# Kernel tuning notes

Measured on AMD Instinct MI355X. Metric: run time of the kernel, lower is better.

Reference implementation:

```python
import jax, jax.numpy as jnp
import numpy as np

# ---- static config (matches init_kwargs) ----
IMG = 56        # num_patches = image_size // patch_size = 112 // 2
WIN = 7         # window_size
SHIFT = 3       # shift_size
C = 256         # projection_dim
H = 8           # num_heads
DH = C // H     # head dim = 32
S = WIN * WIN   # tokens per window = 49
NY = IMG // WIN # windows per side = 8
NW = NY * NY    # windows per image = 64
NMLP = 1024
EPS = 1e-5
SCALE = DH ** (-0.5)


def _relative_position_index():
    ch, cw = np.meshgrid(np.arange(WIN), np.arange(WIN), indexing='ij')
    coords = np.stack([ch, cw]).reshape(2, -1)                 # [2, S]
    rel = coords[:, :, None] - coords[:, None, :]              # [2, S, S]
    rel = rel.transpose(1, 2, 0) + (WIN - 1)                   # [S, S, 2]
    idx = rel[:, :, 0] * (2 * WIN - 1) + rel[:, :, 1]          # [S, S]
    return idx.reshape(-1)                                     # [S*S]

REL_IDX = jnp.asarray(_relative_position_index(), dtype=jnp.int32)


def _attn_mask():
    # Faithful replication of the module's mask construction (incl. the empty
    h_slices = (slice(0, -WIN), slice(-WIN, -SHIFT), slice(-SHIFT, None))
    w_slices = (slice(0, -WIN), slice(-WIN, -WIN), slice(-SHIFT, None))
    m = np.zeros((IMG, IMG), dtype=np.float32)
    count = 0
    for hs in h_slices:
        for ws in w_slices:
            m[hs, ws] = count
            count += 1
    mw = m.reshape(NY, WIN, NY, WIN).transpose(0, 2, 1, 3).reshape(NW, S)
    diff = mw[:, None, :] - mw[:, :, None]
    return np.where(diff != 0, -100.0, 0.0).astype(np.float32)  # [NW, S, S]

ATTN_MASK = jnp.asarray(_attn_mask())


def _layernorm(x, gamma, beta):
    mu = jnp.mean(x, axis=-1, keepdims=True)
    var = jnp.mean(jnp.square(x - mu), axis=-1, keepdims=True)
    return (x - mu) * jax.lax.rsqrt(var + EPS) * gamma + beta


def setup_inputs() -> dict:
    key = jax.random.key(0)
    ks = jax.random.split(key, 12)
    B = 32
    s = lambda fan: 1.0 / np.sqrt(fan)
    return {
        'x': jax.random.normal(ks[0], (B, IMG * IMG, C), dtype=jnp.float32),
        'norm_gamma': jnp.ones((C,), jnp.float32),
        'norm_beta': jnp.zeros((C,), jnp.float32),
        'qkv_w': jax.random.normal(ks[1], (C, 3 * C), jnp.float32) * s(C),
        'qkv_b': jnp.zeros((3 * C,), jnp.float32),
        'proj_w': jax.random.normal(ks[2], (C, C), jnp.float32) * s(C),
        'proj_b': jnp.zeros((C,), jnp.float32),
        'rel_bias_table': jax.random.truncated_normal(ks[3], -2.0, 2.0, ((2 * WIN - 1) ** 2, H), jnp.float32) * 0.02,
        'mlp_w1': jax.random.normal(ks[4], (C, NMLP), jnp.float32) * s(C),
        'mlp_b1': jnp.zeros((NMLP,), jnp.float32),
        'mlp_w2': jax.random.normal(ks[5], (NMLP, C), jnp.float32) * s(NMLP),
        'mlp_b2': jnp.zeros((C,), jnp.float32),
    }


def reference(x, norm_gamma, norm_beta, qkv_w, qkv_b, proj_w, proj_b,
              rel_bias_table, mlp_w1, mlp_b1, mlp_w2, mlp_b2):
    B = x.shape[0]
    # ---- shifted-window attention block ----
    shortcut = x
    xn = _layernorm(x, norm_gamma, norm_beta).reshape(B, IMG, IMG, C)
    shifted = jnp.roll(xn, shift=(-SHIFT, -SHIFT), axis=(1, 2))
    # window partition -> [B*NW, S, C]
    xw = shifted.reshape(B, NY, WIN, NY, WIN, C).transpose(0, 1, 3, 2, 4, 5)
    xw = xw.reshape(B * NW, S, C)
    qkv = xw @ qkv_w + qkv_b                                    # [BnW, S, 3C]
    qkv = qkv.reshape(B * NW, S, 3, H, DH).transpose(2, 0, 3, 1, 4)
    q, k, v = qkv[0] * SCALE, qkv[1], qkv[2]                    # [BnW, H, S, DH]
    attn = jnp.einsum('whsd,whtd->whst', q, k)                  # [BnW, H, S, S]
    bias = rel_bias_table[REL_IDX].reshape(S, S, H).transpose(2, 0, 1)
    attn = attn + bias[None]
    attn = attn.reshape(B, NW, H, S, S) + ATTN_MASK[None, :, None]
    attn = jax.nn.softmax(attn.reshape(B * NW, H, S, S), axis=-1)
    out = jnp.einsum('whst,whtd->wshd', attn, v).reshape(B * NW, S, C)
    out = out @ proj_w + proj_b
    # window reverse + unshift
    out = out.reshape(B, NY, NY, WIN, WIN, C).transpose(0, 1, 3, 2, 4, 5)
    out = out.reshape(B, IMG, IMG, C)
    out = jnp.roll(out, shift=(SHIFT, SHIFT), axis=(1, 2)).reshape(B, IMG * IMG, C)
    x = shortcut + out
    # ---- MLP block (same LayerNorm weights reused, as in original) ----
    shortcut2 = x
    xn2 = _layernorm(x, norm_gamma, norm_beta)
    h = jax.nn.gelu(xn2 @ mlp_w1 + mlp_b1, approximate=False)
    h = h @ mlp_w2 + mlp_b2
    return shortcut2 + h
```

## Files before the change

kernel.cpp:

```cpp
#include <hip/hip_runtime.h>
#include <math.h>

#define IMG   56
#define WINSZ 7
#define SHIFTSZ 3
#define CDIM  256
#define NH    8
#define DH    32
#define SEQ   49
#define NYW   8
#define NWIN  64
#define NMLP  1024
#define BATCH 32
#define NTOK  (BATCH*IMG*IMG)
#define BNW   (BATCH*NWIN)
#define SZT   ((size_t)NTOK*CDIM)
#define QSCALE 0.17677669529663687f
#define EPSLN 1e-5f

typedef __attribute__((ext_vector_type(8))) short short8;
typedef __attribute__((ext_vector_type(4))) float f32x4;

__device__ __forceinline__ float bf2f(unsigned short u) {
    union { unsigned i; float f; } c; c.i = ((unsigned)u) << 16; return c.f;
}
__device__ __forceinline__ unsigned short f2bf(float f) {
    union { float f; unsigned i; } c; c.f = f;
    unsigned r = c.i + 0x7fffu + ((c.i >> 16) & 1u);
    return (unsigned short)(r >> 16);
}

__device__ __forceinline__ float gelu_f(float v) {
    float u = v * 0.70710678118654752f;
    float x = fabsf(u);
    float t = __builtin_amdgcn_rcpf(fmaf(0.3275911f, x, 1.0f));
    float e = __expf(-u * u);
    float p = fmaf(1.061405429f, t, -1.453152027f);
    p = fmaf(p, t, 1.421413741f);
    p = fmaf(p, t, -0.284496736f);
    p = fmaf(p, t, 0.254829592f);
    float er = 1.0f - p * t * e;
    er = copysignf(er, u);
    return 0.5f * v * (1.0f + er);
}

#define GLL16(gp, lp) __builtin_amdgcn_global_load_lds( \
    (__attribute__((address_space(1))) void*)(gp),      \
    (__attribute__((address_space(3))) void*)(lp), 16, 0, 0)

__global__ __launch_bounds__(256) void wtrans(const float* __restrict__ in,
                                              unsigned short* __restrict__ out,
                                              int K, int N) {
    int idx = blockIdx.x * 256 + threadIdx.x;
    if (idx >= K * N) return;
    int n = idx / K, k = idx - n * K;
    out[idx] = f2bf(in[(size_t)k * N + n]);
}

template<int WINDOWED>
__global__ __launch_bounds__(256) void ln_kernel(const float* __restrict__ x,
                                                 const float* __restrict__ gamma,
                                                 const float* __restrict__ beta,
                                                 unsigned short* __restrict__ out) {
    int wave = threadIdx.x >> 6;
    int lane = threadIdx.x & 63;
    int tok  = blockIdx.x * 4 + wave;
    int src  = tok;
    if (WINDOWED) {
        int b  = tok / (NWIN * SEQ);
        int r  = tok - b * (NWIN * SEQ);
        int wl = r / SEQ, s = r - wl * SEQ;
        int wy = wl >> 3, wx = wl & 7;
        int i  = s / WINSZ, j = s - i * WINSZ;
        int hp = wy * WINSZ + i + SHIFTSZ; if (hp >= IMG) hp -= IMG;
        int wp = wx * WINSZ + j + SHIFTSZ; if (wp >= IMG) wp -= IMG;
        src = b * (IMG * IMG) + hp * IMG + wp;
    }
    float4 v = *(const float4*)(x + (size_t)src * CDIM + lane * 4);
    float sum = v.x + v.y + v.z + v.w;
    float ss  = v.x*v.x + v.y*v.y + v.z*v.z + v.w*v.w;
#pragma unroll
    for (int off = 32; off; off >>= 1) {
        sum += __shfl_xor(sum, off);
        ss  += __shfl_xor(ss,  off);
    }
    float mu   = sum * (1.0f / CDIM);
    float var  = ss * (1.0f / CDIM) - mu * mu;
    float rstd = rsqrtf(var + EPSLN);
    float4 g  = *(const float4*)(gamma + lane * 4);
    float4 be = *(const float4*)(beta  + lane * 4);
    ushort4 o;
    o.x = f2bf((v.x - mu) * rstd * g.x + be.x);
    o.y = f2bf((v.y - mu) * rstd * g.y + be.y);
    o.z = f2bf((v.z - mu) * rstd * g.z + be.z);
    o.w = f2bf((v.w - mu) * rstd * g.w + be.w);
    *(ushort4*)(out + (size_t)tok * CDIM + lane * 4) = o;
}

#define EPI_QKV  0
#define EPI_PROJ 1
#define EPI_MLP1 2
#define EPI_MLP2 3

template<int EPI>
__global__ __launch_bounds__(256)
void gemm_bt(const unsigned short* __restrict__ A,
             const unsigned short* __restrict__ Bt,
             int K,
             const float* __restrict__ bias,
             const float* __restrict__ resin,
             float* __restrict__ outF,
             unsigned short* __restrict__ outH) {
    __shared__ __align__(16) unsigned short As[128 * 32];
    __shared__ __align__(16) unsigned short Bs[128 * 32];
    int tid  = threadIdx.x;
    int lane = tid & 63, wave = tid >> 6;
    int q4   = lane >> 4, l16 = lane & 15;
    int wm   = wave >> 1, wn = wave & 1;
    int rowBase = blockIdx.y * 128;
    int colBase = blockIdx.x * 128;

    f32x4 acc[4][4];
#pragma unroll
    for (int i = 0; i < 4; i++)
#pragma unroll
        for (int j = 0; j < 4; j++) acc[i][j] = (f32x4){0.f, 0.f, 0.f, 0.f};

    const unsigned short* Ab = A  + (size_t)rowBase * K;
    const unsigned short* Bb = Bt + (size_t)colBase * K;

    int r0 = wave * 32;
    int ra = r0 + (lane >> 2);
    int rb = ra + 16;
    int ca = (lane & 3) ^ ((ra >> 1) & 3);
    int cb = (lane & 3) ^ ((rb >> 1) & 3);
    const size_t off1 = (size_t)ra * K + ca * 8;
    const size_t off2 = (size_t)rb * K + cb * 8;
    unsigned short* ldsA1 = &As[r0 * 32];
    unsigned short* ldsA2 = &As[(r0 + 16) * 32];
    unsigned short* ldsB1 = &Bs[r0 * 32];
    unsigned short* ldsB2 = &Bs[(r0 + 16) * 32];

    for (int k0 = 0; k0 < K; k0 += 32) {
        __syncthreads();
        GLL16(Ab + off1 + k0, ldsA1);
        GLL16(Ab + off2 + k0, ldsA2);
        GLL16(Bb + off1 + k0, ldsB1);
        GLL16(Bb + off2 + k0, ldsB2);
        __syncthreads();
        short8 af[4], bf[4];
#pragma unroll
        for (int mi = 0; mi < 4; mi++) {
            int r = wm * 64 + mi * 16 + l16;
            af[mi] = *(const short8*)&As[r * 32 + ((q4 ^ ((r >> 1) & 3)) * 8)];
        }
#pragma unroll
        for (int ni = 0; ni < 4; ni++) {
            int r = wn * 64 + ni * 16 + l16;
            bf[ni] = *(const short8*)&Bs[r * 32 + ((q4 ^ ((r >> 1) & 3)) * 8)];
        }
#pragma unroll
        for (int mi = 0; mi < 4; mi++)
#pragma unroll
            for (int ni = 0; ni < 4; ni++)
                acc[mi][ni] = __builtin_amdgcn_mfma_f32_16x16x32_bf16(
                    bf[ni], af[mi], acc[mi][ni], 0, 0, 0);
    }

    int mb = rowBase + wm * 64;
    int nb = colBase + wn * 64;
    float4 bias4[4];
#pragma unroll
    for (int ni = 0; ni < 4; ni++)
        bias4[ni] = *(const float4*)(bias + nb + ni * 16 + q4 * 4);

    if (EPI == EPI_QKV) {
        int three = colBase >> 8;
#pragma unroll
        for (int mi = 0; mi < 4; mi++) {
            int m = mb + mi * 16 + l16;
            int w = m / SEQ, s = m - w * SEQ;
#pragma unroll
            for (int ni = 0; ni < 4; ni++) {
                int n0 = nb + ni * 16 + q4 * 4;
                int hh = (n0 >> 5) & 7, dd0 = n0 & 31;
                const float* bp = (const float*)&bias4[ni];
                if (three == 2) {
#pragma unroll
                    for (int r = 0; r < 4; r++)
                        outH[2 * SZT + (((size_t)(w * NH + hh)) * DH + dd0 + r) * 64 + s] =
                            f2bf(acc[mi][ni][r] + bp[r]);
                } else {
                    float sc = (three == 0) ? QSCALE : 1.0f;
                    ushort4 o;
                    o.x = f2bf((acc[mi][ni][0] + bp[0]) * sc);
                    o.y = f2bf((acc[mi][ni][1] + bp[1]) * sc);
                    o.z = f2bf((acc[mi][ni][2] + bp[2]) * sc);
                    o.w = f2bf((acc[mi][ni][3] + bp[3]) * sc);
                    *(ushort4*)(outH + (size_t)three * SZT +
                                (((size_t)(w * NH + hh)) * SEQ + s) * DH + dd0) = o;
                }
            }
        }
    } else if (EPI == EPI_PROJ) {
#pragma unroll
        for (int mi = 0; mi < 4; mi++) {
            int m = mb + mi * 16 + l16;
            int w = m / SEQ, s = m - w * SEQ;
            int b = w >> 6, wl = w & 63;
            int wy = wl >> 3, wx = wl & 7;
            int ii = s / WINSZ, jj = s - ii * WINSZ;
            int hp = wy * WINSZ + ii + SHIFTSZ; if (hp >= IMG) hp -= IMG;
            int wp = wx * WINSZ + jj + SHIFTSZ; if (wp >= IMG) wp -= IMG;
            size_t tok = (size_t)b * (IMG * IMG) + hp * IMG + wp;
#pragma unroll
            for (int ni = 0; ni < 4; ni++) {
                int n0 = nb + ni * 16 + q4 * 4;
                float4 res = *(const float4*)(resin + tok * CDIM + n0);
                float4 o;
                o.x = acc[mi][ni][0] + bias4[ni].x + res.x;
                o.y = acc[mi][ni][1] + bias4[ni].y + res.y;
                o.z = acc[mi][ni][2] + bias4[ni].z + res.z;
                o.w = acc[mi][ni][3] + bias4[ni].w + res.w;
                *(float4*)(outF + tok * CDIM + n0) = o;
            }
        }
    } else if (EPI == EPI_MLP1) {
#pragma unroll
        for (int mi = 0; mi < 4; mi++) {
            int m = mb + mi * 16 + l16;
#pragma unroll
            for (int ni = 0; ni < 4; ni++) {
                int n0 = nb + ni * 16 + q4 * 4;
                ushort4 o;
                o.x = f2bf(gelu_f(acc[mi][ni][0] + bias4[ni].x));
                o.y = f2bf(gelu_f(acc[mi][ni][1] + bias4[ni].y));
                o.z = f2bf(gelu_f(acc[mi][ni][2] + bias4[ni].z));
                o.w = f2bf(gelu_f(acc[mi][ni][3] + bias4[ni].w));
                *(ushort4*)(outH + (size_t)m * NMLP + n0) = o;
            }
        }
    } else {
#pragma unroll
        for (int mi = 0; mi < 4; mi++) {
            int m = mb + mi * 16 + l16;
#pragma unroll
            for (int ni = 0; ni < 4; ni++) {
                int n0 = nb + ni * 16 + q4 * 4;
                float4 res = *(const float4*)(resin + (size_t)m * CDIM + n0);
                float4 o;
                o.x = acc[mi][ni][0] + bias4[ni].x + res.x;
                o.y = acc[mi][ni][1] + bias4[ni].y + res.y;
                o.z = acc[mi][ni][2] + bias4[ni].z + res.z;
                o.w = acc[mi][ni][3] + bias4[ni].w + res.w;
                *(float4*)(outF + (size_t)m * CDIM + n0) = o;
            }
        }
    }
}

__global__ __launch_bounds__(256) void attn_mfma(const unsigned short* __restrict__ qb,
                                                 const unsigned short* __restrict__ kb,
                                                 const unsigned short* __restrict__ vT,
                                                 const float* __restrict__ rel_tab,
                                                 unsigned short* __restrict__ outp) {
    __shared__ __align__(16) unsigned short Pl[4][64 * 64];
    __shared__ float tab[4][169];
    int tid  = threadIdx.x;
    int wave = tid >> 6, lane = tid & 63;
    int q4   = lane >> 4, l16 = lane & 15;
    int job  = blockIdx.x * 4 + wave;
    int w    = job >> 3, h = job & 7;

    for (int i = lane; i < 169; i += 64) tab[wave][i] = rel_tab[i * NH + h];

    const unsigned short* qg = qb + (size_t)(w * NH + h) * SEQ * DH;
    const unsigned short* kg = kb + (size_t)(w * NH + h) * SEQ * DH;
    short8 aq[4], bk[4];
#pragma unroll
    for (int mi = 0; mi < 4; mi++)
        aq[mi] = *(const short8*)(qg + (mi * 16 + l16) * DH + q4 * 8);
#pragma unroll
    for (int ni = 0; ni < 4; ni++)
        bk[ni] = *(const short8*)(kg + (ni * 16 + l16) * DH + q4 * 8);

    f32x4 acc[4][4];
#pragma unroll
    for (int i = 0; i < 4; i++)
#pragma unroll
        for (int j = 0; j < 4; j++) acc[i][j] = (f32x4){0.f, 0.f, 0.f, 0.f};
#pragma unroll
    for (int mi = 0; mi < 4; mi++)
#pragma unroll
        for (int ni = 0; ni < 4; ni++)
            acc[mi][ni] = __builtin_amdgcn_mfma_f32_16x16x32_bf16(
                aq[mi], bk[ni], acc[mi][ni], 0, 0, 0);

    int wl = w & 63;
    int wy = wl >> 3, wx = wl & 7;
    bool edge = (wy == 7) || (wx == 7);

    int itv[4], jtv[4], ltv[4];
#pragma unroll
    for (int ni = 0; ni < 4; ni++) {
        int t  = ni * 16 + l16;
        int it = (t * 37) >> 8;
        int jt = t - it * 7;
        itv[ni] = it; jtv[ni] = jt;
        int lab;
        if (wx == 7 && jt < 4) lab = 0;
        else {
            int lh = (wy == 7) ? ((it < 4) ? 1 : 2) : 0;
            lab = lh * 3 + ((wx == 7) ? 2 : 0);
        }
        ltv[ni] = lab;
    }

    float rinv[4][4];
#pragma unroll
    for (int mi = 0; mi < 4; mi++) {
#pragma unroll
        for (int r = 0; r < 4; r++) {
            int s  = mi * 16 + q4 * 4 + r;
            int is = (s * 37) >> 8;
            int js = s - is * 7;
            int lab_s;
            if (wx == 7 && js < 4) lab_s = 0;
            else {
                int lh = (wy == 7) ? ((is < 4) ? 1 : 2) : 0;
                lab_s = lh * 3 + ((wx == 7) ? 2 : 0);
            }
            float vv[4];
#pragma unroll
            for (int ni = 0; ni < 4; ni++) {
                int t = ni * 16 + l16;
                float a = acc[mi][ni][r];
                if (t < SEQ) {
                    int idx = (is - itv[ni] + 6) * 13 + (js - jtv[ni] + 6);
                    idx = idx < 0 ? 0 : (idx > 168 ? 168 : idx);
                    a += tab[wave][idx];
                    if (edge && lab_s != ltv[ni]) a -= 100.0f;
                } else {
                    a = -1e30f;
                }
                vv[ni] = a;
            }
            float mx = fmaxf(fmaxf(vv[0], vv[1]), fmaxf(vv[2], vv[3]));
#pragma unroll
            for (int off = 1; off < 16; off <<= 1) mx = fmaxf(mx, __shfl_xor(mx, off));
            float sm = 0.0f;
            unsigned short pb[4];
#pragma unroll
            for (int ni = 0; ni < 4; ni++) {
                float p = __expf(vv[ni] - mx);
                sm += p;
                pb[ni] = f2bf(p);
            }
#pragma unroll
            for (int off = 1; off < 16; off <<= 1) sm += __shfl_xor(sm, off);
            rinv[mi][r] = 1.0f / sm;
#pragma unroll
            for (int ni = 0; ni < 4; ni++) {
                int t  = ni * 16 + l16;
                int kbk = t >> 3, j = t & 7;
                Pl[wave][s * 64 + ((kbk ^ (s & 7)) * 8) + j] = pb[ni];
            }
        }
    }
    __syncthreads();

    short8 pa[4][2];
#pragma unroll
    for (int mi = 0; mi < 4; mi++)
#pragma unroll
        for (int ks = 0; ks < 2; ks++) {
            int m  = mi * 16 + l16;
            int kbk = ks * 4 + q4;
            pa[mi][ks] = *(const short8*)&Pl[wave][m * 64 + ((kbk ^ (m & 7)) * 8)];
        }
    const unsigned short* vg = vT + (size_t)(w * NH + h) * DH * 64;
    short8 bv[2][2];
#pragma unroll
    for (int n2 = 0; n2 < 2; n2++)
#pragma unroll
        for (int ks = 0; ks < 2; ks++)
            bv[n2][ks] = *(const short8*)(vg + (n2 * 16 + l16) * 64 + ks * 32 + q4 * 8);

    f32x4 o[4][2];
#pragma unroll
    for (int mi = 0; mi < 4; mi++)
#pragma unroll
        for (int n2 = 0; n2 < 2; n2++) o[mi][n2] = (f32x4){0.f, 0.f, 0.f, 0.f};
#pragma unroll
    for (int ks = 0; ks < 2; ks++)
#pragma unroll
        for (int mi = 0; mi < 4; mi++)
#pragma unroll
            for (int n2 = 0; n2 < 2; n2++)
                o[mi][n2] = __builtin_amdgcn_mfma_f32_16x16x32_bf16(
                    pa[mi][ks], bv[n2][ks], o[mi][n2], 0, 0, 0);

#pragma unroll
    for (int mi = 0; mi < 4; mi++)
#pragma unroll
        for (int r = 0; r < 4; r++) {
            int s = mi * 16 + q4 * 4 + r;
            if (s < SEQ) {
#pragma unroll
                for (int n2 = 0; n2 < 2; n2++) {
                    int d = n2 * 16 + l16;
                    outp[((size_t)w * SEQ + s) * CDIM + h * DH + d] =
                        f2bf(o[mi][n2][r] * rinv[mi][r]);
                }
            }
        }
}

extern "C" void kernel_launch(void* const* d_in, const int* in_sizes, int n_in,
                              void* d_out, int out_size, void* d_ws, size_t ws_size,
                              hipStream_t stream) {
    const float* x      = (const float*)d_in[0];
    const float* gamma  = (const float*)d_in[1];
    const float* beta   = (const float*)d_in[2];
    const float* qkv_w  = (const float*)d_in[3];
    const float* qkv_b  = (const float*)d_in[4];
    const float* proj_w = (const float*)d_in[5];
    const float* proj_b = (const float*)d_in[6];
    const float* rel_t  = (const float*)d_in[7];
    const float* mlp_w1 = (const float*)d_in[8];
    const float* mlp_b1 = (const float*)d_in[9];
    const float* mlp_w2 = (const float*)d_in[10];
    const float* mlp_b2 = (const float*)d_in[11];
    float* outp = (float*)d_out;

    const size_t VTSZ = (size_t)BNW * NH * DH * 64;
    unsigned short* xw_bf   = (unsigned short*)d_ws;
    unsigned short* qkv_bf  = xw_bf + SZT;
    unsigned short* attn_bf = qkv_bf + 2 * SZT + VTSZ;
    float*          y1      = (float*)(attn_bf + SZT);
    unsigned short* wt_bf   = (unsigned short*)(y1 + SZT);
    unsigned short* h_bf    = qkv_bf;

    unsigned short* qkvW  = wt_bf;
    unsigned short* projW = qkvW  + 768 * 256;
    unsigned short* mlp1W = projW + 256 * 256;
    unsigned short* mlp2W = mlp1W + 1024 * 256;

    wtrans<<<(768 * 256 + 255) / 256, 256, 0, stream>>>(qkv_w, qkvW, CDIM, 3 * CDIM);
    wtrans<<<(256 * 256 + 255) / 256, 256, 0, stream>>>(proj_w, projW, CDIM, CDIM);
    wtrans<<<(1024 * 256 + 255) / 256, 256, 0, stream>>>(mlp_w1, mlp1W, CDIM, NMLP);
    wtrans<<<(256 * 1024 + 255) / 256, 256, 0, stream>>>(mlp_w2, mlp2W, NMLP, CDIM);

    ln_kernel<1><<<NTOK / 4, 256, 0, stream>>>(x, gamma, beta, xw_bf);
    gemm_bt<EPI_QKV><<<dim3(6, NTOK / 128), 256, 0, stream>>>(
        xw_bf, qkvW, CDIM, qkv_b, nullptr, nullptr, qkv_bf);
    attn_mfma<<<BNW * NH / 4, 256, 0, stream>>>(
        qkv_bf, qkv_bf + SZT, qkv_bf + 2 * SZT, rel_t, attn_bf);
    gemm_bt<EPI_PROJ><<<dim3(2, NTOK / 128), 256, 0, stream>>>(
        attn_bf, projW, CDIM, proj_b, x, y1, nullptr);
    ln_kernel<0><<<NTOK / 4, 256, 0, stream>>>(y1, gamma, beta, xw_bf);
    gemm_bt<EPI_MLP1><<<dim3(8, NTOK / 128), 256, 0, stream>>>(
        xw_bf, mlp1W, CDIM, mlp_b1, nullptr, nullptr, h_bf);
    gemm_bt<EPI_MLP2><<<dim3(2, NTOK / 128), 256, 0, stream>>>(
        h_bf, mlp2W, NMLP, mlp_b2, y1, outp, nullptr);
}
```

Baseline: 754.8 us.

## Double-buffer LDS tiles in bf16 GEMM to overlap global loads with MFMA

The GEMM main loop now uses two LDS buffers for the A and B tiles. The next K-slice is loaded while MFMAs run on the current one, and there is one barrier per iteration instead of two. Launch bounds also request 4 blocks per CU, which caps register usage. This hides global-to-LDS latency at the cost of doubled shared memory (32KB per block) and possible register pressure from the occupancy hint.

After: 718.3 us. -4.8%, faster.

```diff
diff --git a/kernel.cpp b/kernel.cpp
--- a/kernel.cpp
+++ b/kernel.cpp
@@ -103,7 +103,7 @@
 #define EPI_MLP2 3
 
 template<int EPI>
-__global__ __launch_bounds__(256)
+__global__ __launch_bounds__(256, 4)
 void gemm_bt(const unsigned short* __restrict__ A,
              const unsigned short* __restrict__ Bt,
              int K,
@@ -111,8 +111,8 @@
              const float* __restrict__ resin,
              float* __restrict__ outF,
              unsigned short* __restrict__ outH) {
-    __shared__ __align__(16) unsigned short As[128 * 32];
-    __shared__ __align__(16) unsigned short Bs[128 * 32];
+    __shared__ __align__(16) unsigned short As[2][128 * 32];
+    __shared__ __align__(16) unsigned short Bs[2][128 * 32];
     int tid  = threadIdx.x;
     int lane = tid & 63, wave = tid >> 6;
     int q4   = lane >> 4, l16 = lane & 15;
@@ -136,28 +136,24 @@
     int cb = (lane & 3) ^ ((rb >> 1) & 3);
     const size_t off1 = (size_t)ra * K + ca * 8;
     const size_t off2 = (size_t)rb * K + cb * 8;
-    unsigned short* ldsA1 = &As[r0 * 32];
-    unsigned short* ldsA2 = &As[(r0 + 16) * 32];
-    unsigned short* ldsB1 = &Bs[r0 * 32];
-    unsigned short* ldsB2 = &Bs[(r0 + 16) * 32];
-
-    for (int k0 = 0; k0 < K; k0 += 32) {
-        __syncthreads();
-        GLL16(Ab + off1 + k0, ldsA1);
-        GLL16(Ab + off2 + k0, ldsA2);
-        GLL16(Bb + off1 + k0, ldsB1);
-        GLL16(Bb + off2 + k0, ldsB2);
-        __syncthreads();
+
+    auto stage = [&](int c, int k0) {
+        GLL16(Ab + off1 + k0, &As[c][r0 * 32]);
+        GLL16(Ab + off2 + k0, &As[c][(r0 + 16) * 32]);
+        GLL16(Bb + off1 + k0, &Bs[c][r0 * 32]);
+        GLL16(Bb + off2 + k0, &Bs[c][(r0 + 16) * 32]);
+    };
+    auto compute = [&](int c) {
         short8 af[4], bf[4];
 #pragma unroll
         for (int mi = 0; mi < 4; mi++) {
             int r = wm * 64 + mi * 16 + l16;
-            af[mi] = *(const short8*)&As[r * 32 + ((q4 ^ ((r >> 1) & 3)) * 8)];
+            af[mi] = *(const short8*)&As[c][r * 32 + ((q4 ^ ((r >> 1) & 3)) * 8)];
         }
 #pragma unroll
         for (int ni = 0; ni < 4; ni++) {
             int r = wn * 64 + ni * 16 + l16;
-            bf[ni] = *(const short8*)&Bs[r * 32 + ((q4 ^ ((r >> 1) & 3)) * 8)];
+            bf[ni] = *(const short8*)&Bs[c][r * 32 + ((q4 ^ ((r >> 1) & 3)) * 8)];
         }
 #pragma unroll
         for (int mi = 0; mi < 4; mi++)
@@ -165,7 +161,19 @@
             for (int ni = 0; ni < 4; ni++)
                 acc[mi][ni] = __builtin_amdgcn_mfma_f32_16x16x32_bf16(
                     bf[ni], af[mi], acc[mi][ni], 0, 0, 0);
-    }
+    };
+
+    int nt = K >> 5;
+    stage(0, 0);
+    __syncthreads();
+    int cur = 0;
+    for (int t = 0; t < nt - 1; ++t) {
+        stage(cur ^ 1, (t + 1) * 32);
+        compute(cur);
+        __syncthreads();
+        cur ^= 1;
+    }
+    compute(cur);
 
     int mb = rowBase + wm * 64;
     int nb = colBase + wn * 64;
```
